# Optimization experiments

Hardware: AMD Instinct MI355X
Metric: run time of the kernel (lower is better)

The kernel has to match this reference:

```python
import jax, jax.numpy as jnp
import numpy as np

B, N, D, OUT = 8192, 256, 128, 10  # batch, input_dim (sites), bond_dim, output_dim
LOCAL = 2  # local physical dimension (hardcoded in source)


def setup_inputs() -> dict:
    key = jax.random.key(0)
    ks = jax.random.split(key, 6)
    scale = 1.0 / np.sqrt(D)  # stable variant of source's 0.1 init (keeps 256-site product O(1))
    x = jax.random.normal(ks[0], (B, N), dtype=jnp.float32)
    first = jax.random.normal(ks[1], (1, LOCAL, D), dtype=jnp.float32) * scale   # site 0: (1,2,D)
    mid = jax.random.normal(ks[2], (N - 2, D, LOCAL, D), dtype=jnp.float32) * scale  # sites 1..N-2
    last = jax.random.normal(ks[3], (D, LOCAL, 1), dtype=jnp.float32) * scale    # site N-1: (D,2,1)
    w = jax.random.normal(ks[4], (OUT, 1), dtype=jnp.float32) * 0.1  # nn.Linear(1, OUT) weight
    b = jnp.zeros((OUT,), dtype=jnp.float32)                          # nn.Linear(1, OUT) bias
    return {"x": x, "first": first, "mid": mid, "last": last, "w": w, "b": b}


def _feature_map(x):
    # per-sample min/max normalization over the feature axis, then (cos, sin) embedding
    x_min = jnp.min(x, axis=1, keepdims=True)
    x_max = jnp.max(x, axis=1, keepdims=True)
    x_norm = (x - x_min) / (x_max - x_min + 1e-6)
    ang = (np.pi / 2) * x_norm
    return jnp.stack([jnp.cos(ang), jnp.sin(ang)], axis=2)  # [B, N, 2]


def reference(x, first, mid, last, w, b):
    phi = _feature_map(x)  # [B, N, 2]
    # site 0: left[b, r] = sum_d first[0, d, r] * phi[b, 0, d]
    left = jnp.einsum('dr,bd->br', first[0], phi[:, 0])  # [B, D]
    # sites 1..N-2 via scan: left <- sum_{l,d} left[b,l] * M[l,d,r] * phi[b,i,d]
    phi_mid = jnp.swapaxes(phi[:, 1:-1], 0, 1)  # [N-2, B, 2]

    def step(left, inputs):
        M, p = inputs  # M: [D, 2, D], p: [B, 2]
        left = jnp.einsum('bl,ldr,bd->br', left, M, p)
        return left, None

    left, _ = jax.lax.scan(step, left, (mid, phi_mid))  # [B, D]
    # last site: scalar[b] = sum_{l,d} left[b,l] * last[l,d,0] * phi[b,N-1,d]
    scalar = jnp.einsum('bl,ld,bd->b', left, last[:, :, 0], phi[:, -1])  # [B]
    # nn.Linear(1, OUT): logits = scalar * w^T + b
    logits = scalar[:, None] * w[:, 0][None, :] + b  # [B, OUT]
    return logits
```

## Files before the change

### kernel.cpp

```cpp
#include <hip/hip_runtime.h>


typedef _Float16 v8h __attribute__((ext_vector_type(8)));
typedef _Float16 h2  __attribute__((ext_vector_type(2)));
typedef float    v4f __attribute__((ext_vector_type(4)));

#define PI_HALF 1.5707963267948966f
#define SITE_U4 4096
#define TOFF_U4 (254*4096)

union U4H8 { uint4 u; v8h h; };

__device__ __forceinline__ v4f mfma16h(uint4 a, uint4 b, v4f c){
  U4H8 ua, ub; ua.u = a; ub.u = b;
  return __builtin_amdgcn_mfma_f32_16x16x32_f16(ua.h, ub.h, c, 0, 0, 0);
}
__device__ __forceinline__ unsigned pack2h(float lo, float hi){
  h2 p; p[0] = (_Float16)lo; p[1] = (_Float16)hi;
  return __builtin_bit_cast(unsigned, p);
}

__global__ __launch_bounds__(256) void repack_mid(const float* __restrict__ mid,
                                                  unsigned short* __restrict__ wsB){
  const int bid = blockIdx.x;
  if (bid < 1016){
    int idx  = bid * 256 + threadIdx.x;
    int lg   = idx & 15;
    int nt   = (idx >> 4) & 7;
    int kt   = (idx >> 7) & 3;
    int d    = (idx >> 9) & 1;
    int site = idx >> 10;
    int q    = lg >> 2;
    int n0   = 16*nt + 4*(lg & 3);
    const float* src = mid + ((size_t)(site*128 + 32*kt + 8*q)*2 + d)*128 + n0;
    float V[8][4];
    #pragma unroll
    for (int j = 0; j < 8; ++j){
      float4 a = *(const float4*)(src + (size_t)j*256);
      V[j][0]=a.x; V[j][1]=a.y; V[j][2]=a.z; V[j][3]=a.w;
    }
    uint4* dst = (uint4*)wsB + ((((size_t)site*2 + d)*4 + kt)*8 + nt)*64
               + 16*q + 4*(lg & 3);
    #pragma unroll
    for (int t = 0; t < 4; ++t){
      uint4 o;
      o.x = pack2h(V[0][t], V[1][t]);
      o.y = pack2h(V[2][t], V[3][t]);
      o.z = pack2h(V[4][t], V[5][t]);
      o.w = pack2h(V[6][t], V[7][t]);
      dst[t] = o;
    }
  } else {
    int idx  = (bid - 1016) * 256 + threadIdx.x;
    int lg   = idx & 15;
    int kt   = (idx >> 4) & 3;
    int am   = (idx >> 6) & 7;
    int d    = (idx >> 9) & 1;
    int site = idx >> 10;
    int q    = lg >> 2;
    int m0   = 16*am + 4*(lg & 3);
    int k0   = 32*kt + 8*q;
    uint4* dst = (uint4*)wsB + TOFF_U4
               + ((((size_t)site*2 + d)*8 + am)*4 + kt)*64 + 16*q + 4*(lg & 3);
    #pragma unroll
    for (int mp = 0; mp < 4; ++mp){
      const float* src = mid + ((size_t)((site*128 + m0 + mp)*2) + d)*128 + k0;
      float4 a = *(const float4*)(src);
      float4 b = *(const float4*)(src + 4);
      uint4 o;
      o.x = pack2h(a.x, a.y);
      o.y = pack2h(a.z, a.w);
      o.z = pack2h(b.x, b.y);
      o.w = pack2h(b.z, b.w);
      dst[mp] = o;
    }
  }
}

__global__ __launch_bounds__(512, 2) void mps_main(
    const float* __restrict__ x,
    const float* __restrict__ first,
    const unsigned short* __restrict__ wsBv,
    const float* __restrict__ lastw,
    const float* __restrict__ wlin,
    const float* __restrict__ blin,
    float* __restrict__ out)
{
  __shared__ unsigned phiT[256*36];
  __shared__ unsigned Af[2*2*4*64*4];
  __shared__ unsigned Rf[2*4*2*64*4];
  __shared__ float Rcomb[128*33];
  __shared__ float scal[32];

  const int tid  = threadIdx.x;
  const int gblk = blockIdx.x;
  const int w    = tid >> 6;
  const int lane = tid & 63;
  const int r    = lane & 15;
  const int q    = lane >> 4;
  const int rh   = r >> 3;
  const int rowbase = gblk * 32;
  const int physL = lane ^ ((lane >> 3) & 7);

  {
    const int row = tid >> 4;
    const int c0  = (tid & 15) * 16;
    const float4* xp = (const float4*)(x + (size_t)(rowbase + row) * 256 + c0);
    float xv[16];
    float vmin = 3.0e38f, vmax = -3.0e38f;
    #pragma unroll
    for (int c = 0; c < 4; ++c){
      float4 u = xp[c];
      xv[c*4+0] = u.x; xv[c*4+1] = u.y; xv[c*4+2] = u.z; xv[c*4+3] = u.w;
      vmin = fminf(vmin, fminf(fminf(u.x,u.y), fminf(u.z,u.w)));
      vmax = fmaxf(vmax, fmaxf(fmaxf(u.x,u.y), fmaxf(u.z,u.w)));
    }
    #pragma unroll
    for (int m = 1; m < 16; m <<= 1){
      vmin = fminf(vmin, __shfl_xor(vmin, m));
      vmax = fmaxf(vmax, __shfl_xor(vmax, m));
    }
    const float sc = PI_HALF / (vmax - vmin + 1e-6f);
    #pragma unroll
    for (int j = 0; j < 16; ++j){
      float a = (xv[j] - vmin) * sc;
      phiT[(c0 + j)*36 + row] = pack2h(__cosf(a), __sinf(a));
    }
  }
  __syncthreads();

  uint4 B0[16], B1[16];
  if (w < 4){
    const uint4* bp = (const uint4*)wsBv;
    #pragma unroll
    for (int d = 0; d < 2; ++d)
      #pragma unroll
      for (int kt = 0; kt < 4; ++kt)
        #pragma unroll
        for (int nb = 0; nb < 2; ++nb)
          B0[(d*4+kt)*2+nb] = bp[(size_t)((d*4 + kt)*8 + 2*w + nb)*64 + lane];
  } else {
    const int ww = w - 4;
    const uint4* bp = (const uint4*)wsBv + TOFF_U4 + (size_t)253 * SITE_U4;
    #pragma unroll
    for (int d = 0; d < 2; ++d)
      #pragma unroll
      for (int mtl = 0; mtl < 2; ++mtl)
        #pragma unroll
        for (int kt = 0; kt < 4; ++kt)
          B0[(d*2+mtl)*4+kt] = bp[(size_t)((d*8 + 2*ww + mtl)*4 + kt)*64 + lane];
  }

  if (w < 4){
    float f0[8], f1[8];
    #pragma unroll
    for (int j = 0; j < 8; ++j){
      int l = 32*w + 8*q + j;
      f0[j] = first[l]; f1[j] = first[128 + l];
    }
    #pragma unroll
    for (int mt = 0; mt < 2; ++mt){
      h2 ph0 = __builtin_bit_cast(h2, phiT[0*36 + 16*mt + r]);
      const float c0 = (float)ph0[0], s0 = (float)ph0[1];
      uint4 o;
      o.x = pack2h(f0[0]*c0 + f1[0]*s0, f0[1]*c0 + f1[1]*s0);
      o.y = pack2h(f0[2]*c0 + f1[2]*s0, f0[3]*c0 + f1[3]*s0);
      o.z = pack2h(f0[4]*c0 + f1[4]*s0, f0[5]*c0 + f1[5]*s0);
      o.w = pack2h(f0[6]*c0 + f1[6]*s0, f0[7]*c0 + f1[7]*s0);
      *(uint4*)&Af[((mt*4 + w)*64 + physL)*4] = o;
    }
  } else {
    const int ww = w - 4;
    float g0[8], g1[8];
    #pragma unroll
    for (int j = 0; j < 8; ++j){
      int rr = 32*ww + 8*q + j;
      float2 gg = *(const float2*)(lastw + 2*rr);
      g0[j] = gg.x; g1[j] = gg.y;
    }
    #pragma unroll
    for (int nt = 0; nt < 2; ++nt){
      h2 p5 = __builtin_bit_cast(h2, phiT[255*36 + 16*nt + r]);
      const float cb = (float)p5[0], sb = (float)p5[1];
      uint4 o;
      o.x = pack2h(g0[0]*cb + g1[0]*sb, g0[1]*cb + g1[1]*sb);
      o.y = pack2h(g0[2]*cb + g1[2]*sb, g0[3]*cb + g1[3]*sb);
      o.z = pack2h(g0[4]*cb + g1[4]*sb, g0[5]*cb + g1[5]*sb);
      o.w = pack2h(g0[6]*cb + g1[6]*sb, g0[7]*cb + g1[7]*sb);
      *(uint4*)&Rf[((ww*2 + nt)*64 + physL)*4] = o;
    }
  }

  auto body = [&](int t, uint4 (&Fc)[16], uint4 (&Fn)[16]){
    __syncthreads();
    float vf[2][2][4];

    if (w < 4){
      {
        const int soff = (t < 126) ? (t + 1) : 0;
        const uint4* bp = (const uint4*)wsBv + (size_t)soff * SITE_U4;
        #pragma unroll
        for (int d = 0; d < 2; ++d)
          #pragma unroll
          for (int kt = 0; kt < 4; ++kt)
            #pragma unroll
            for (int nb = 0; nb < 2; ++nb)
              Fn[(d*4+kt)*2+nb] = bp[(size_t)((d*4 + kt)*8 + 2*w + nb)*64 + lane];
      }
      v4f ac0[2][2] = {};
      v4f ac1[2][2] = {};
      const unsigned* Ab = &Af[(t & 1) * 2048];
      #pragma unroll
      for (int kt = 0; kt < 4; ++kt){
        uint4 a0 = *(const uint4*)&Ab[((0*4 + kt)*64 + physL)*4];
        uint4 a1 = *(const uint4*)&Ab[((1*4 + kt)*64 + physL)*4];
        #pragma unroll
        for (int nb = 0; nb < 2; ++nb){
          ac0[0][nb] = mfma16h(a0, Fc[(0*4+kt)*2+nb], ac0[0][nb]);
          ac0[1][nb] = mfma16h(a1, Fc[(0*4+kt)*2+nb], ac0[1][nb]);
          ac1[0][nb] = mfma16h(a0, Fc[(1*4+kt)*2+nb], ac1[0][nb]);
          ac1[1][nb] = mfma16h(a1, Fc[(1*4+kt)*2+nb], ac1[1][nb]);
        }
      }
      if (t < 126){
        unsigned short* Wb = (unsigned short*)&Af[((t+1) & 1) * 2048];
        #pragma unroll
        for (int mt = 0; mt < 2; ++mt){
          uint4 phiu = *(const uint4*)&phiT[(t+1)*36 + 16*mt + 4*q];
          const unsigned pr[4] = {phiu.x, phiu.y, phiu.z, phiu.w};
          #pragma unroll
          for (int nb = 0; nb < 2; ++nb){
            const int S0 = 32*nb + 16*rh + 4*q;
            const int X  = 4*nb + 2*rh + (q >> 1);
            #pragma unroll
            for (int reg = 0; reg < 4; ++reg){
              h2 ph = __builtin_bit_cast(h2, pr[reg]);
              float v = (float)ph[0]*ac0[mt][nb][reg]
                      + (float)ph[1]*ac1[mt][nb][reg];
              Wb[((mt*4 + w)*64 + ((S0 + reg) ^ X))*8 + (r & 7)] =
                  __builtin_bit_cast(unsigned short, (_Float16)v);
            }
          }
        }
      } else {
        #pragma unroll
        for (int mt = 0; mt < 2; ++mt){
          uint4 phiu = *(const uint4*)&phiT[127*36 + 16*mt + 4*q];
          const unsigned pr[4] = {phiu.x, phiu.y, phiu.z, phiu.w};
          #pragma unroll
          for (int nb = 0; nb < 2; ++nb)
            #pragma unroll
            for (int reg = 0; reg < 4; ++reg){
              h2 ph = __builtin_bit_cast(h2, pr[reg]);
              vf[mt][nb][reg] = (float)ph[0]*ac0[mt][nb][reg]
                              + (float)ph[1]*ac1[mt][nb][reg];
            }
        }
      }
    } else {
      const int ww = w - 4;
      {
        const int soff = (t < 126) ? (252 - t) : 253;
        const uint4* bp = (const uint4*)wsBv + TOFF_U4 + (size_t)soff * SITE_U4;
        #pragma unroll
        for (int d = 0; d < 2; ++d)
          #pragma unroll
          for (int mtl = 0; mtl < 2; ++mtl)
            #pragma unroll
            for (int kt = 0; kt < 4; ++kt)
              Fn[(d*2+mtl)*4+kt] = bp[(size_t)((d*8 + 2*ww + mtl)*4 + kt)*64 + lane];
      }
      v4f ac0[2][2] = {};
      v4f ac1[2][2] = {};
      const unsigned* Rb = &Rf[(t & 1) * 2048];
      #pragma unroll
      for (int kt = 0; kt < 4; ++kt){
        uint4 b0 = *(const uint4*)&Rb[((kt*2 + 0)*64 + physL)*4];
        uint4 b1 = *(const uint4*)&Rb[((kt*2 + 1)*64 + physL)*4];
        #pragma unroll
        for (int mtl = 0; mtl < 2; ++mtl){
          ac0[mtl][0] = mfma16h(Fc[(0*2+mtl)*4+kt], b0, ac0[mtl][0]);
          ac0[mtl][1] = mfma16h(Fc[(0*2+mtl)*4+kt], b1, ac0[mtl][1]);
          ac1[mtl][0] = mfma16h(Fc[(1*2+mtl)*4+kt], b0, ac1[mtl][0]);
          ac1[mtl][1] = mfma16h(Fc[(1*2+mtl)*4+kt], b1, ac1[mtl][1]);
        }
      }
      const int ps = 254 - t;
      if (t < 126){
        unsigned short* Wr = (unsigned short*)&Rf[((t+1) & 1) * 2048];
        #pragma unroll
        for (int nb = 0; nb < 2; ++nb){
          h2 ph = __builtin_bit_cast(h2, phiT[ps*36 + 16*nb + r]);
          const float cb = (float)ph[0], sb = (float)ph[1];
          #pragma unroll
          for (int mtl = 0; mtl < 2; ++mtl){
            const int S0 = 32*mtl + 16*(q >> 1) + r;
            const int phys = S0 ^ ((S0 >> 3) & 7);
            #pragma unroll
            for (int reg = 0; reg < 4; ++reg){
              float v = cb*ac0[mtl][nb][reg] + sb*ac1[mtl][nb][reg];
              Wr[((ww*2 + nb)*64 + phys)*8 + ((4*q + reg) & 7)] =
                  __builtin_bit_cast(unsigned short, (_Float16)v);
            }
          }
        }
      } else {
        #pragma unroll
        for (int nb = 0; nb < 2; ++nb){
          h2 ph = __builtin_bit_cast(h2, phiT[ps*36 + 16*nb + r]);
          const float cb = (float)ph[0], sb = (float)ph[1];
          #pragma unroll
          for (int mtl = 0; mtl < 2; ++mtl)
            #pragma unroll
            for (int reg = 0; reg < 4; ++reg){
              float v = cb*ac0[mtl][nb][reg] + sb*ac1[mtl][nb][reg];
              int l = 32*ww + 16*mtl + 4*q + reg;
              Rcomb[l*33 + 16*nb + r] = v;
            }
        }
      }
    }

    if (t == 126){
      if (tid < 32) scal[tid] = 0.0f;
      __syncthreads();
      if (w < 4){
        float p[2][4] = {};
        #pragma unroll
        for (int mt = 0; mt < 2; ++mt)
          #pragma unroll
          for (int nb = 0; nb < 2; ++nb){
            const int l = 32*w + 16*nb + r;
            #pragma unroll
            for (int reg = 0; reg < 4; ++reg)
              p[mt][reg] += vf[mt][nb][reg] * Rcomb[l*33 + 16*mt + 4*q + reg];
          }
        #pragma unroll
        for (int m = 1; m < 16; m <<= 1)
          #pragma unroll
          for (int mt = 0; mt < 2; ++mt)
            #pragma unroll
            for (int reg = 0; reg < 4; ++reg)
              p[mt][reg] += __shfl_xor(p[mt][reg], m);
        if (r == 0){
          #pragma unroll
          for (int mt = 0; mt < 2; ++mt)
            #pragma unroll
            for (int reg = 0; reg < 4; ++reg)
              atomicAdd(&scal[16*mt + 4*q + reg], p[mt][reg]);
        }
      }
      __syncthreads();
      for (int t2 = tid; t2 < 320; t2 += 512){
        int bb = t2 / 10, o = t2 - bb*10;
        out[(size_t)(rowbase + bb)*10 + o] = scal[bb]*wlin[o] + blin[o];
      }
    }
  };

  #pragma unroll 1
  for (int t = 0; t < 126; t += 2){
    body(t,     B0, B1);
    body(t + 1, B1, B0);
  }
  body(126, B0, B1);
}

extern "C" void kernel_launch(void* const* d_in, const int* in_sizes, int n_in,
                              void* d_out, int out_size, void* d_ws, size_t ws_size,
                              hipStream_t stream){
  (void)in_sizes; (void)n_in; (void)out_size; (void)ws_size;
  const float* x     = (const float*)d_in[0];
  const float* first = (const float*)d_in[1];
  const float* mid   = (const float*)d_in[2];
  const float* lastw = (const float*)d_in[3];
  const float* wlin  = (const float*)d_in[4];
  const float* blin  = (const float*)d_in[5];
  float* o            = (float*)d_out;
  unsigned short* wsB = (unsigned short*)d_ws;

  hipLaunchKernelGGL(repack_mid, dim3(2032), dim3(256), 0, stream, mid, wsB);
  hipLaunchKernelGGL(mps_main,   dim3(256),  dim3(512), 0, stream,
                     x, first, wsB, lastw, wlin, blin, o);
}
```

Measured before the change: 269.7 us.

## Split each chain's MFMA work across twice as many waves with 1024-thread blocks

Measured after the change: 274.2 us. About the same (+1.7%).

```diff
diff --git a/kernel.cpp b/kernel.cpp
--- a/kernel.cpp
+++ b/kernel.cpp
@@ -7,7 +7,7 @@
 
 #define PI_HALF 1.5707963267948966f
 #define SITE_U4 4096
-#define TOFF_U4 (254*4096)
+#define TOFF_U4 (127*4096)
 
 union U4H8 { uint4 u; v8h h; };
 
@@ -19,11 +19,14 @@
   h2 p; p[0] = (_Float16)lo; p[1] = (_Float16)hi;
   return __builtin_bit_cast(unsigned, p);
 }
+__device__ __forceinline__ unsigned short f16b(float v){
+  return __builtin_bit_cast(unsigned short, (_Float16)v);
+}
 
 __global__ __launch_bounds__(256) void repack_mid(const float* __restrict__ mid,
                                                   unsigned short* __restrict__ wsB){
   const int bid = blockIdx.x;
-  if (bid < 1016){
+  if (bid < 508){
     int idx  = bid * 256 + threadIdx.x;
     int lg   = idx & 15;
     int nt   = (idx >> 4) & 7;
@@ -51,17 +54,18 @@
       dst[t] = o;
     }
   } else {
-    int idx  = (bid - 1016) * 256 + threadIdx.x;
+    int idx  = (bid - 508) * 256 + threadIdx.x;
     int lg   = idx & 15;
     int kt   = (idx >> 4) & 3;
     int am   = (idx >> 6) & 7;
     int d    = (idx >> 9) & 1;
-    int site = idx >> 10;
+    int srel = idx >> 10;
+    int site = 127 + srel;
     int q    = lg >> 2;
     int m0   = 16*am + 4*(lg & 3);
     int k0   = 32*kt + 8*q;
     uint4* dst = (uint4*)wsB + TOFF_U4
-               + ((((size_t)site*2 + d)*8 + am)*4 + kt)*64 + 16*q + 4*(lg & 3);
+               + ((((size_t)srel*2 + d)*8 + am)*4 + kt)*64 + 16*q + 4*(lg & 3);
     #pragma unroll
     for (int mp = 0; mp < 4; ++mp){
       const float* src = mid + ((size_t)((site*128 + m0 + mp)*2) + d)*128 + k0;
@@ -77,7 +81,7 @@
   }
 }
 
-__global__ __launch_bounds__(512, 2) void mps_main(
+__global__ __launch_bounds__(1024, 4) void mps_main(
     const float* __restrict__ x,
     const float* __restrict__ first,
     const unsigned short* __restrict__ wsBv,
@@ -87,8 +91,8 @@
     float* __restrict__ out)
 {
   __shared__ unsigned phiT[256*36];
-  __shared__ unsigned Af[2*2*4*64*4];
-  __shared__ unsigned Rf[2*4*2*64*4];
+  __shared__ unsigned Af[2*8*64*4];
+  __shared__ unsigned Rf[2*8*64*4];
   __shared__ float Rcomb[128*33];
   __shared__ float scal[32];
 
@@ -103,255 +107,215 @@
   const int physL = lane ^ ((lane >> 3) & 7);
 
   {
-    const int row = tid >> 4;
-    const int c0  = (tid & 15) * 16;
+    const int row = tid >> 5;
+    const int c0  = (tid & 31) * 8;
     const float4* xp = (const float4*)(x + (size_t)(rowbase + row) * 256 + c0);
-    float xv[16];
+    float xv[8];
     float vmin = 3.0e38f, vmax = -3.0e38f;
     #pragma unroll
-    for (int c = 0; c < 4; ++c){
+    for (int c = 0; c < 2; ++c){
       float4 u = xp[c];
       xv[c*4+0] = u.x; xv[c*4+1] = u.y; xv[c*4+2] = u.z; xv[c*4+3] = u.w;
       vmin = fminf(vmin, fminf(fminf(u.x,u.y), fminf(u.z,u.w)));
       vmax = fmaxf(vmax, fmaxf(fmaxf(u.x,u.y), fmaxf(u.z,u.w)));
     }
     #pragma unroll
-    for (int m = 1; m < 16; m <<= 1){
+    for (int m = 1; m < 32; m <<= 1){
       vmin = fminf(vmin, __shfl_xor(vmin, m));
       vmax = fmaxf(vmax, __shfl_xor(vmax, m));
     }
     const float sc = PI_HALF / (vmax - vmin + 1e-6f);
     #pragma unroll
-    for (int j = 0; j < 16; ++j){
+    for (int j = 0; j < 8; ++j){
       float a = (xv[j] - vmin) * sc;
       phiT[(c0 + j)*36 + row] = pack2h(__cosf(a), __sinf(a));
     }
   }
   __syncthreads();
 
-  uint4 B0[16], B1[16];
-  if (w < 4){
+  uint4 F0[8], F1[8];
+  if (w < 8){
+    const int mt = w >> 2, kt = w & 3;
+    float f0[8], f1[8];
+    #pragma unroll
+    for (int j = 0; j < 8; ++j){
+      int l = 32*kt + 8*q + j;
+      f0[j] = first[l]; f1[j] = first[128 + l];
+    }
+    h2 p0 = __builtin_bit_cast(h2, phiT[0*36 + 16*mt + r]);
+    const float c0 = (float)p0[0], s0 = (float)p0[1];
+    uint4 o;
+    o.x = pack2h(f0[0]*c0 + f1[0]*s0, f0[1]*c0 + f1[1]*s0);
+    o.y = pack2h(f0[2]*c0 + f1[2]*s0, f0[3]*c0 + f1[3]*s0);
+    o.z = pack2h(f0[4]*c0 + f1[4]*s0, f0[5]*c0 + f1[5]*s0);
+    o.w = pack2h(f0[6]*c0 + f1[6]*s0, f0[7]*c0 + f1[7]*s0);
+    *(uint4*)&Af[((mt*4 + kt)*64 + physL)*4] = o;
     const uint4* bp = (const uint4*)wsBv;
     #pragma unroll
     for (int d = 0; d < 2; ++d)
       #pragma unroll
-      for (int kt = 0; kt < 4; ++kt)
-        #pragma unroll
-        for (int nb = 0; nb < 2; ++nb)
-          B0[(d*4+kt)*2+nb] = bp[(size_t)((d*4 + kt)*8 + 2*w + nb)*64 + lane];
+      for (int kk = 0; kk < 4; ++kk)
+        F0[d*4+kk] = bp[(size_t)((d*4 + kk)*8 + w)*64 + lane];
   } else {
-    const int ww = w - 4;
-    const uint4* bp = (const uint4*)wsBv + TOFF_U4 + (size_t)253 * SITE_U4;
+    const int ww = w - 8;
+    const int kt = ww >> 1, nt = ww & 1;
+    const int n  = 16*nt + r;
+    h2 p5 = __builtin_bit_cast(h2, phiT[255*36 + n]);
+    const float cb = (float)p5[0], sb = (float)p5[1];
+    uint4 o; unsigned ow[4];
+    #pragma unroll
+    for (int jp = 0; jp < 4; ++jp){
+      const int k = 32*kt + 8*q + 2*jp;
+      float2 g0 = *(const float2*)(lastw + 2*k);
+      float2 g1 = *(const float2*)(lastw + 2*(k+1));
+      ow[jp] = pack2h(g0.x*cb + g0.y*sb, g1.x*cb + g1.y*sb);
+    }
+    o.x=ow[0]; o.y=ow[1]; o.z=ow[2]; o.w=ow[3];
+    *(uint4*)&Rf[((kt*2 + nt)*64 + physL)*4] = o;
+    const uint4* bp = (const uint4*)wsBv + TOFF_U4 + (size_t)126 * SITE_U4;
     #pragma unroll
     for (int d = 0; d < 2; ++d)
       #pragma unroll
-      for (int mtl = 0; mtl < 2; ++mtl)
-        #pragma unroll
-        for (int kt = 0; kt < 4; ++kt)
-          B0[(d*2+mtl)*4+kt] = bp[(size_t)((d*8 + 2*ww + mtl)*4 + kt)*64 + lane];
+      for (int kk = 0; kk < 4; ++kk)
+        F0[d*4+kk] = bp[(size_t)((d*8 + ww)*4 + kk)*64 + lane];
   }
 
-  if (w < 4){
-    float f0[8], f1[8];
-    #pragma unroll
-    for (int j = 0; j < 8; ++j){
-      int l = 32*w + 8*q + j;
-      f0[j] = first[l]; f1[j] = first[128 + l];
-    }
-    #pragma unroll
-    for (int mt = 0; mt < 2; ++mt){
-      h2 ph0 = __builtin_bit_cast(h2, phiT[0*36 + 16*mt + r]);
-      const float c0 = (float)ph0[0], s0 = (float)ph0[1];
-      uint4 o;
-      o.x = pack2h(f0[0]*c0 + f1[0]*s0, f0[1]*c0 + f1[1]*s0);
-      o.y = pack2h(f0[2]*c0 + f1[2]*s0, f0[3]*c0 + f1[3]*s0);
-      o.z = pack2h(f0[4]*c0 + f1[4]*s0, f0[5]*c0 + f1[5]*s0);
-      o.w = pack2h(f0[6]*c0 + f1[6]*s0, f0[7]*c0 + f1[7]*s0);
-      *(uint4*)&Af[((mt*4 + w)*64 + physL)*4] = o;
-    }
-  } else {
-    const int ww = w - 4;
-    float g0[8], g1[8];
-    #pragma unroll
-    for (int j = 0; j < 8; ++j){
-      int rr = 32*ww + 8*q + j;
-      float2 gg = *(const float2*)(lastw + 2*rr);
-      g0[j] = gg.x; g1[j] = gg.y;
-    }
-    #pragma unroll
-    for (int nt = 0; nt < 2; ++nt){
-      h2 p5 = __builtin_bit_cast(h2, phiT[255*36 + 16*nt + r]);
-      const float cb = (float)p5[0], sb = (float)p5[1];
-      uint4 o;
-      o.x = pack2h(g0[0]*cb + g1[0]*sb, g0[1]*cb + g1[1]*sb);
-      o.y = pack2h(g0[2]*cb + g1[2]*sb, g0[3]*cb + g1[3]*sb);
-      o.z = pack2h(g0[4]*cb + g1[4]*sb, g0[5]*cb + g1[5]*sb);
-      o.w = pack2h(g0[6]*cb + g1[6]*sb, g0[7]*cb + g1[7]*sb);
-      *(uint4*)&Rf[((ww*2 + nt)*64 + physL)*4] = o;
-    }
-  }
-
-  auto body = [&](int t, uint4 (&Fc)[16], uint4 (&Fn)[16]){
+  auto body = [&](int t, uint4 (&Fc)[8], uint4 (&Fn)[8]){
     __syncthreads();
-    float vf[2][2][4];
-
-    if (w < 4){
+
+    if (w < 8){
       {
         const int soff = (t < 126) ? (t + 1) : 0;
         const uint4* bp = (const uint4*)wsBv + (size_t)soff * SITE_U4;
         #pragma unroll
         for (int d = 0; d < 2; ++d)
           #pragma unroll
-          for (int kt = 0; kt < 4; ++kt)
-            #pragma unroll
-            for (int nb = 0; nb < 2; ++nb)
-              Fn[(d*4+kt)*2+nb] = bp[(size_t)((d*4 + kt)*8 + 2*w + nb)*64 + lane];
-      }
-      v4f ac0[2][2] = {};
-      v4f ac1[2][2] = {};
+          for (int kk = 0; kk < 4; ++kk)
+            Fn[d*4+kk] = bp[(size_t)((d*4 + kk)*8 + w)*64 + lane];
+      }
+      v4f ac0[2] = {};
+      v4f ac1[2] = {};
       const unsigned* Ab = &Af[(t & 1) * 2048];
       #pragma unroll
       for (int kt = 0; kt < 4; ++kt){
         uint4 a0 = *(const uint4*)&Ab[((0*4 + kt)*64 + physL)*4];
         uint4 a1 = *(const uint4*)&Ab[((1*4 + kt)*64 + physL)*4];
-        #pragma unroll
-        for (int nb = 0; nb < 2; ++nb){
-          ac0[0][nb] = mfma16h(a0, Fc[(0*4+kt)*2+nb], ac0[0][nb]);
-          ac0[1][nb] = mfma16h(a1, Fc[(0*4+kt)*2+nb], ac0[1][nb]);
-          ac1[0][nb] = mfma16h(a0, Fc[(1*4+kt)*2+nb], ac1[0][nb]);
-          ac1[1][nb] = mfma16h(a1, Fc[(1*4+kt)*2+nb], ac1[1][nb]);
-        }
+        ac0[0] = mfma16h(a0, Fc[0*4+kt], ac0[0]);
+        ac0[1] = mfma16h(a1, Fc[0*4+kt], ac0[1]);
+        ac1[0] = mfma16h(a0, Fc[1*4+kt], ac1[0]);
+        ac1[1] = mfma16h(a1, Fc[1*4+kt], ac1[1]);
       }
       if (t < 126){
         unsigned short* Wb = (unsigned short*)&Af[((t+1) & 1) * 2048];
+        const int X  = 4*(w & 1) + 2*rh + (q >> 1);
+        const int S0 = 32*(w & 1) + 16*rh + 4*q;
         #pragma unroll
         for (int mt = 0; mt < 2; ++mt){
           uint4 phiu = *(const uint4*)&phiT[(t+1)*36 + 16*mt + 4*q];
           const unsigned pr[4] = {phiu.x, phiu.y, phiu.z, phiu.w};
-          #pragma unroll
-          for (int nb = 0; nb < 2; ++nb){
-            const int S0 = 32*nb + 16*rh + 4*q;
-            const int X  = 4*nb + 2*rh + (q >> 1);
-            #pragma unroll
-            for (int reg = 0; reg < 4; ++reg){
-              h2 ph = __builtin_bit_cast(h2, pr[reg]);
-              float v = (float)ph[0]*ac0[mt][nb][reg]
-                      + (float)ph[1]*ac1[mt][nb][reg];
-              Wb[((mt*4 + w)*64 + ((S0 + reg) ^ X))*8 + (r & 7)] =
-                  __builtin_bit_cast(unsigned short, (_Float16)v);
-            }
+          const int base16 = (mt*4 + (w >> 1))*512;
+          #pragma unroll
+          for (int reg = 0; reg < 4; ++reg){
+            h2 ph = __builtin_bit_cast(h2, pr[reg]);
+            float v = (float)ph[0]*ac0[mt][reg] + (float)ph[1]*ac1[mt][reg];
+            Wb[base16 + ((S0 + reg) ^ X)*8 + (r & 7)] = f16b(v);
           }
         }
       } else {
+        float vf[2][4];
         #pragma unroll
         for (int mt = 0; mt < 2; ++mt){
           uint4 phiu = *(const uint4*)&phiT[127*36 + 16*mt + 4*q];
           const unsigned pr[4] = {phiu.x, phiu.y, phiu.z, phiu.w};
           #pragma unroll
-          for (int nb = 0; nb < 2; ++nb)
+          for (int reg = 0; reg < 4; ++reg){
+            h2 ph = __builtin_bit_cast(h2, pr[reg]);
+            vf[mt][reg] = (float)ph[0]*ac0[mt][reg] + (float)ph[1]*ac1[mt][reg];
+          }
+        }
+        if (tid < 32) scal[tid] = 0.0f;
+        __syncthreads();
+        float p[2][4] = {};
+        const int l = 16*w + r;
+        #pragma unroll
+        for (int mt = 0; mt < 2; ++mt)
+          #pragma unroll
+          for (int reg = 0; reg < 4; ++reg)
+            p[mt][reg] = vf[mt][reg] * Rcomb[l*33 + 16*mt + 4*q + reg];
+        #pragma unroll
+        for (int m = 1; m < 16; m <<= 1)
+          #pragma unroll
+          for (int mt = 0; mt < 2; ++mt)
             #pragma unroll
-            for (int reg = 0; reg < 4; ++reg){
-              h2 ph = __builtin_bit_cast(h2, pr[reg]);
-              vf[mt][nb][reg] = (float)ph[0]*ac0[mt][nb][reg]
-                              + (float)ph[1]*ac1[mt][nb][reg];
-            }
+            for (int reg = 0; reg < 4; ++reg)
+              p[mt][reg] += __shfl_xor(p[mt][reg], m);
+        if (r == 0){
+          #pragma unroll
+          for (int mt = 0; mt < 2; ++mt)
+            #pragma unroll
+            for (int reg = 0; reg < 4; ++reg)
+              atomicAdd(&scal[16*mt + 4*q + reg], p[mt][reg]);
         }
       }
     } else {
-      const int ww = w - 4;
+      const int ww = w - 8;
       {
-        const int soff = (t < 126) ? (252 - t) : 253;
-        const uint4* bp = (const uint4*)wsBv + TOFF_U4 + (size_t)soff * SITE_U4;
+        const int srel = (t < 126) ? (125 - t) : 0;
+        const uint4* bp = (const uint4*)wsBv + TOFF_U4 + (size_t)srel * SITE_U4;
         #pragma unroll
         for (int d = 0; d < 2; ++d)
           #pragma unroll
-          for (int mtl = 0; mtl < 2; ++mtl)
-            #pragma unroll
-            for (int kt = 0; kt < 4; ++kt)
-              Fn[(d*2+mtl)*4+kt] = bp[(size_t)((d*8 + 2*ww + mtl)*4 + kt)*64 + lane];
-      }
-      v4f ac0[2][2] = {};
-      v4f ac1[2][2] = {};
+          for (int kk = 0; kk < 4; ++kk)
+            Fn[d*4+kk] = bp[(size_t)((d*8 + ww)*4 + kk)*64 + lane];
+      }
+      v4f ac0[2] = {};
+      v4f ac1[2] = {};
       const unsigned* Rb = &Rf[(t & 1) * 2048];
       #pragma unroll
       for (int kt = 0; kt < 4; ++kt){
         uint4 b0 = *(const uint4*)&Rb[((kt*2 + 0)*64 + physL)*4];
         uint4 b1 = *(const uint4*)&Rb[((kt*2 + 1)*64 + physL)*4];
-        #pragma unroll
-        for (int mtl = 0; mtl < 2; ++mtl){
-          ac0[mtl][0] = mfma16h(Fc[(0*2+mtl)*4+kt], b0, ac0[mtl][0]);
-          ac0[mtl][1] = mfma16h(Fc[(0*2+mtl)*4+kt], b1, ac0[mtl][1]);
-          ac1[mtl][0] = mfma16h(Fc[(1*2+mtl)*4+kt], b0, ac1[mtl][0]);
-          ac1[mtl][1] = mfma16h(Fc[(1*2+mtl)*4+kt], b1, ac1[mtl][1]);
-        }
+        ac0[0] = mfma16h(Fc[0*4+kt], b0, ac0[0]);
+        ac0[1] = mfma16h(Fc[0*4+kt], b1, ac0[1]);
+        ac1[0] = mfma16h(Fc[1*4+kt], b0, ac1[0]);
+        ac1[1] = mfma16h(Fc[1*4+kt], b1, ac1[1]);
       }
       const int ps = 254 - t;
       if (t < 126){
         unsigned short* Wr = (unsigned short*)&Rf[((t+1) & 1) * 2048];
-        #pragma unroll
-        for (int nb = 0; nb < 2; ++nb){
-          h2 ph = __builtin_bit_cast(h2, phiT[ps*36 + 16*nb + r]);
+        const int X = 4*(ww & 1) + 2*(q >> 1) + rh;
+        const int S = (32*(ww & 1) + 16*(q >> 1) + r) ^ X;
+        #pragma unroll
+        for (int nt = 0; nt < 2; ++nt){
+          h2 ph = __builtin_bit_cast(h2, phiT[ps*36 + 16*nt + r]);
           const float cb = (float)ph[0], sb = (float)ph[1];
-          #pragma unroll
-          for (int mtl = 0; mtl < 2; ++mtl){
-            const int S0 = 32*mtl + 16*(q >> 1) + r;
-            const int phys = S0 ^ ((S0 >> 3) & 7);
-            #pragma unroll
-            for (int reg = 0; reg < 4; ++reg){
-              float v = cb*ac0[mtl][nb][reg] + sb*ac1[mtl][nb][reg];
-              Wr[((ww*2 + nb)*64 + phys)*8 + ((4*q + reg) & 7)] =
-                  __builtin_bit_cast(unsigned short, (_Float16)v);
-            }
+          const int base = ((ww >> 1)*2 + nt)*512 + S*8 + 4*(q & 1);
+          #pragma unroll
+          for (int reg = 0; reg < 4; ++reg){
+            float v = cb*ac0[nt][reg] + sb*ac1[nt][reg];
+            Wr[base + reg] = f16b(v);
           }
         }
       } else {
         #pragma unroll
-        for (int nb = 0; nb < 2; ++nb){
-          h2 ph = __builtin_bit_cast(h2, phiT[ps*36 + 16*nb + r]);
+        for (int nt = 0; nt < 2; ++nt){
+          h2 ph = __builtin_bit_cast(h2, phiT[128*36 + 16*nt + r]);
           const float cb = (float)ph[0], sb = (float)ph[1];
           #pragma unroll
-          for (int mtl = 0; mtl < 2; ++mtl)
-            #pragma unroll
-            for (int reg = 0; reg < 4; ++reg){
-              float v = cb*ac0[mtl][nb][reg] + sb*ac1[mtl][nb][reg];
-              int l = 32*ww + 16*mtl + 4*q + reg;
-              Rcomb[l*33 + 16*nb + r] = v;
-            }
-        }
+          for (int reg = 0; reg < 4; ++reg){
+            float v = cb*ac0[nt][reg] + sb*ac1[nt][reg];
+            const int l = 16*ww + 4*q + reg;
+            Rcomb[l*33 + 16*nt + r] = v;
+          }
+        }
+        if (tid < 32) scal[tid] = 0.0f;
+        __syncthreads();
       }
     }
 
     if (t == 126){
-      if (tid < 32) scal[tid] = 0.0f;
       __syncthreads();
-      if (w < 4){
-        float p[2][4] = {};
-        #pragma unroll
-        for (int mt = 0; mt < 2; ++mt)
-          #pragma unroll
-          for (int nb = 0; nb < 2; ++nb){
-            const int l = 32*w + 16*nb + r;
-            #pragma unroll
-            for (int reg = 0; reg < 4; ++reg)
-              p[mt][reg] += vf[mt][nb][reg] * Rcomb[l*33 + 16*mt + 4*q + reg];
-          }
-        #pragma unroll
-        for (int m = 1; m < 16; m <<= 1)
-          #pragma unroll
-          for (int mt = 0; mt < 2; ++mt)
-            #pragma unroll
-            for (int reg = 0; reg < 4; ++reg)
-              p[mt][reg] += __shfl_xor(p[mt][reg], m);
-        if (r == 0){
-          #pragma unroll
-          for (int mt = 0; mt < 2; ++mt)
-            #pragma unroll
-            for (int reg = 0; reg < 4; ++reg)
-              atomicAdd(&scal[16*mt + 4*q + reg], p[mt][reg]);
-        }
-      }
-      __syncthreads();
-      for (int t2 = tid; t2 < 320; t2 += 512){
+      for (int t2 = tid; t2 < 320; t2 += 1024){
         int bb = t2 / 10, o = t2 - bb*10;
         out[(size_t)(rowbase + bb)*10 + o] = scal[bb]*wlin[o] + blin[o];
       }
@@ -360,10 +324,10 @@
 
   #pragma unroll 1
   for (int t = 0; t < 126; t += 2){
-    body(t,     B0, B1);
-    body(t + 1, B1, B0);
+    body(t,     F0, F1);
+    body(t + 1, F1, F0);
   }
-  body(126, B0, B1);
+  body(126, F0, F1);
 }
 
 extern "C" void kernel_launch(void* const* d_in, const int* in_sizes, int n_in,
@@ -379,7 +343,7 @@
   float* o            = (float*)d_out;
   unsigned short* wsB = (unsigned short*)d_ws;
 
-  hipLaunchKernelGGL(repack_mid, dim3(2032), dim3(256), 0, stream, mid, wsB);
-  hipLaunchKernelGGL(mps_main,   dim3(256),  dim3(512), 0, stream,
+  hipLaunchKernelGGL(repack_mid, dim3(1016), dim3(256),  0, stream, mid, wsB);
+  hipLaunchKernelGGL(mps_main,   dim3(256),  dim3(1024), 0, stream,
                      x, first, wsB, lastw, wlin, blin, o);
 }
```
